# Kernel optimization log

Measured on AMD Instinct MI355X. Metric: run time of the kernel, lower is better.

Reference implementation:

```python
import jax, jax.numpy as jnp
import numpy as np

N_NODES = 50000
N_EDGES = 800000
IN_DIM = 128
HID_DIM = 128
OUT_DIM = 64


def setup_inputs() -> dict:
    key = jax.random.key(0)
    ks = jax.random.split(key, 6)
    x = jax.random.normal(ks[0], (N_NODES, IN_DIM), dtype=jnp.float32)
    edge_index = jax.random.randint(ks[1], (2, N_EDGES), 0, N_NODES, dtype=jnp.int64)
    # per-hop linear weights (torch Linear layout: [out, in], no bias)
    s = 1.0 / np.sqrt(IN_DIM)
    W0 = jax.random.uniform(ks[2], (HID_DIM, IN_DIM), jnp.float32, -s, s)
    W1 = jax.random.uniform(ks[3], (HID_DIM, IN_DIM), jnp.float32, -s, s)
    W2 = jax.random.uniform(ks[4], (HID_DIM, IN_DIM), jnp.float32, -s, s)
    s2 = 1.0 / np.sqrt(HID_DIM * 3)
    Wfc = jax.random.uniform(ks[5], (OUT_DIM, HID_DIM * 3), jnp.float32, -s2, s2)
    return {"x": x, "edge_index": edge_index, "W0": W0, "W1": W1, "W2": W2, "Wfc": Wfc}


def reference(x, edge_index, W0, W1, W2, Wfc):
    N = x.shape[0]
    row, col = edge_index[0], edge_index[1]  # source, target (PyG source_to_target flow)
    # symmetric degree normalization based on in-degree (degree(col, N))
    deg = jax.ops.segment_sum(jnp.ones(row.shape[0], dtype=x.dtype), col, num_segments=N)
    deg_inv_sqrt = jnp.where(deg > 0, jax.lax.rsqrt(jnp.where(deg > 0, deg, 1.0)), 0.0)
    norm = deg_inv_sqrt[row] * deg_inv_sqrt[col]  # [E]
    # NOTE: original code propagates the ORIGINAL x each iteration, so hops 1 and 2
    # both see the 1-hop propagation of x. Faithfully reproduced here.
    px = jax.ops.segment_sum(norm[:, None] * x[row], col, num_segments=N)  # [N, IN_DIM]
    # per-hop linear projections, concat over hops p=[0,1,2]
    h = jnp.concatenate([x @ W0.T, px @ W1.T, px @ W2.T], axis=1)  # [N, 3*HID_DIM]
    return h @ Wfc.T  # [N, OUT_DIM]
```

## Files before the change

kernel.cpp:

```cpp
#include <hip/hip_runtime.h>
#include <hip/hip_bf16.h>

#define N_IN  128
#define N_OUT 64
#define CFB    256
#define MAXNBC 200
#define SLACKC 5120
#define CHUNK  2048
#define PADR   136

typedef __attribute__((ext_vector_type(8))) short short8;
typedef __attribute__((ext_vector_type(4))) float floatx4;

__device__ __forceinline__ unsigned pack_bf16(float a, float b) {
    __hip_bfloat16 ba = __float2bfloat16(a);
    __hip_bfloat16 bb = __float2bfloat16(b);
    unsigned short ua = *(unsigned short*)&ba;
    unsigned short ub = *(unsigned short*)&bb;
    return ((unsigned)ub << 16) | ua;
}
__device__ __forceinline__ float blo(unsigned u) { return __uint_as_float(u << 16); }
__device__ __forceinline__ float bhi(unsigned u) { return __uint_as_float(u & 0xffff0000u); }

__global__ void prep_kernel(const float* __restrict__ W0,
                            const float* __restrict__ W1,
                            const float* __restrict__ W2,
                            const float* __restrict__ Wfc,
                            __hip_bfloat16* __restrict__ CT,
                            int* __restrict__ gcur, int NBC) {
    int t = blockIdx.x * blockDim.x + threadIdx.x;
    if (t < NBC) gcur[t] = t * SLACKC;
    if (t >= 128 * 128) return;
    int n = t >> 7;
    int i = t & 127;
    float a = 0.f;
    if (n < 64) {
        for (int k = 0; k < 128; ++k)
            a += Wfc[n * 384 + k] * W0[k * N_IN + i];
    } else {
        int o = n - 64;
        for (int k = 0; k < 128; ++k)
            a += Wfc[o * 384 + 128 + k] * W1[k * N_IN + i]
               + Wfc[o * 384 + 256 + k] * W2[k * N_IN + i];
    }
    CT[t] = __float2bfloat16(a);
}

__global__ __launch_bounds__(256) void fill_scatter(const int* __restrict__ ei,
                                                    int* __restrict__ gcur,
                                                    unsigned* __restrict__ gsorted,
                                                    int E, int NBC) {
    __shared__ int lcnt[MAXNBC];
    __shared__ int gbase_s[MAXNBC];
    int base = blockIdx.x * CHUNK;
    for (int i = threadIdx.x; i < NBC; i += 256) lcnt[i] = 0;
    __syncthreads();
    int myc[CHUNK / 256];
    #pragma unroll
    for (int q = 0; q < CHUNK / 256; ++q) {
        int e = base + q * 256 + threadIdx.x;
        int c = (e < E) ? ei[E + e] : -1;
        myc[q] = c;
        if (c >= 0) atomicAdd(&lcnt[c >> 8], 1);
    }
    __syncthreads();
    for (int f = threadIdx.x; f < NBC; f += 256) {
        int n = lcnt[f];
        gbase_s[f] = (n > 0) ? atomicAdd(&gcur[f], n) : 0;
    }
    __syncthreads();
    #pragma unroll
    for (int q = 0; q < CHUNK / 256; ++q) {
        int c = myc[q];
        if (c >= 0) {
            int e = base + q * 256 + threadIdx.x;
            unsigned r = (unsigned)ei[e];
            int p = atomicAdd(&gbase_s[c >> 8], 1);
            if (p < ((c >> 8) + 1) * SLACKC)
                gsorted[p] = ((unsigned)c << 16) | r;
        }
    }
}

__global__ __launch_bounds__(256) void sortgemm_kernel(
        const int* __restrict__ gcur,
        const unsigned* __restrict__ gsorted,
        unsigned short* __restrict__ srow,
        int* __restrict__ offs,
        int* __restrict__ cnt,
        float* __restrict__ dis,
        const float* __restrict__ x,
        const __hip_bfloat16* __restrict__ CT,
        float* __restrict__ out,
        __hip_bfloat16* __restrict__ z,
        int N, int NBC) {
    __shared__ __align__(16) char smem[(64 + 128) * PADR * 2];
    int tid = threadIdx.x;

    if (blockIdx.x < NBC) {
        unsigned* ev = (unsigned*)smem;
        int* c256 = (int*)(smem + SLACKC * 4);
        int* cur  = c256 + 256;
        int* ts   = cur + 256;
        int f = blockIdx.x;
        int lo = f * SLACKC;
        int m = min(gcur[f] - lo, SLACKC);
        for (int i = tid; i < m; i += 256) ev[i] = gsorted[lo + i];
        c256[tid] = 0;
        __syncthreads();
        for (int i = tid; i < m; i += 256)
            atomicAdd(&c256[(ev[i] >> 16) & (CFB - 1)], 1);
        __syncthreads();
        int v = c256[tid];
        int xx = v;
        ts[tid] = xx;
        __syncthreads();
        for (int off = 1; off < 256; off <<= 1) {
            int t2 = (tid >= off) ? ts[tid - off] : 0;
            __syncthreads();
            xx += t2; ts[tid] = xx;
            __syncthreads();
        }
        int b = xx - v;
        cur[tid] = b;
        int node = f * CFB + tid;
        if (node < N) {
            offs[node] = lo + b;
            cnt[node] = v;
            dis[node] = v > 0 ? rsqrtf((float)v) : 0.f;
        }
        __syncthreads();
        for (int i = tid; i < m; i += 256) {
            unsigned val = ev[i];
            int cl = (val >> 16) & (CFB - 1);
            int p = atomicAdd(&cur[cl], 1);
            srow[lo + p] = (unsigned short)(val & 0xffffu);
        }
        return;
    }

    unsigned short* xs = (unsigned short*)smem;
    unsigned short* Bs = xs + 64 * PADR;
    int base = (blockIdx.x - NBC) * 64;

    {
        int row = tid >> 2;
        int colq = (tid & 3) * 32;
        int node = base + row;
        unsigned tmp[16];
        if (node < N) {
            const float4* src = (const float4*)(x + (size_t)node * N_IN + colq);
            #pragma unroll
            for (int q = 0; q < 8; ++q) {
                float4 v = src[q];
                tmp[q * 2]     = pack_bf16(v.x, v.y);
                tmp[q * 2 + 1] = pack_bf16(v.z, v.w);
            }
        } else {
            #pragma unroll
            for (int q = 0; q < 16; ++q) tmp[q] = 0u;
        }
        unsigned* dst = (unsigned*)(xs + row * PADR + colq);
        #pragma unroll
        for (int q = 0; q < 16; ++q) dst[q] = tmp[q];
    }
    {
        const unsigned* src = (const unsigned*)CT;
        for (int c = tid; c < 8192; c += 256) {
            int row = c >> 6;
            int col = (c & 63) * 2;
            *(unsigned*)(Bs + row * PADR + col) = src[c];
        }
    }
    __syncthreads();

    int wave = tid >> 6, lane = tid & 63;
    int wm = wave & 1, wn = wave >> 1;
    int quad = lane >> 4, l16 = lane & 15;

    floatx4 acc[2][4];
    #pragma unroll
    for (int mt = 0; mt < 2; ++mt)
        #pragma unroll
        for (int nt = 0; nt < 4; ++nt)
            acc[mt][nt] = (floatx4){0.f, 0.f, 0.f, 0.f};

    #pragma unroll
    for (int kc = 0; kc < 4; ++kc) {
        int kof = kc * 32 + quad * 8;
        short8 afr[2], bfr[4];
        #pragma unroll
        for (int mt = 0; mt < 2; ++mt)
            afr[mt] = *(const short8*)(xs + (wm * 32 + mt * 16 + l16) * PADR + kof);
        #pragma unroll
        for (int nt = 0; nt < 4; ++nt)
            bfr[nt] = *(const short8*)(Bs + (wn * 64 + nt * 16 + l16) * PADR + kof);
        #pragma unroll
        for (int mt = 0; mt < 2; ++mt)
            #pragma unroll
            for (int nt = 0; nt < 4; ++nt)
                acc[mt][nt] = __builtin_amdgcn_mfma_f32_16x16x32_bf16(
                    afr[mt], bfr[nt], acc[mt][nt], 0, 0, 0);
    }

    #pragma unroll
    for (int mt = 0; mt < 2; ++mt) {
        #pragma unroll
        for (int reg = 0; reg < 4; ++reg) {
            int node = base + wm * 32 + mt * 16 + quad * 4 + reg;
            if (node >= N) continue;
            if (wn == 0) {
                #pragma unroll
                for (int nt = 0; nt < 4; ++nt)
                    out[(size_t)node * N_OUT + nt * 16 + l16] = acc[mt][nt][reg];
            } else {
                #pragma unroll
                for (int nt = 0; nt < 4; ++nt)
                    z[((size_t)node << 6) + nt * 16 + l16] =
                        __float2bfloat16(acc[mt][nt][reg]);
            }
        }
    }
}

__global__ __launch_bounds__(256) void gather_kernel(
        const int* __restrict__ offs, const int* __restrict__ cnt,
        const unsigned short* __restrict__ srow, const __hip_bfloat16* __restrict__ z,
        const float* __restrict__ dis, float* __restrict__ out, int N) {
    int node = blockIdx.x * 4 + (threadIdx.x >> 6);
    if (node >= N) return;
    int lane = threadIdx.x & 63;
    int sub  = lane >> 3;
    int jj   = lane & 7;
    int start = offs[node];
    int deg   = cnt[node];
    float a[8] = {0.f, 0.f, 0.f, 0.f, 0.f, 0.f, 0.f, 0.f};
    for (int k0 = 0; k0 < deg; k0 += 64) {
        int m = min(64, deg - k0);
        int idx = 0; float dv = 0.f;
        if (lane < m) {
            idx = (int)srow[start + k0 + lane];
            dv = dis[idx];
        }
        for (int kk = 0; kk < m; kk += 16) {
            int s0 = kk + sub, s1 = kk + 8 + sub;
            int r0 = __shfl(idx, s0); float d0 = __shfl(dv, s0);
            int r1 = __shfl(idx, s1); float d1 = __shfl(dv, s1);
            uint4 u0 = make_uint4(0u, 0u, 0u, 0u), u1 = make_uint4(0u, 0u, 0u, 0u);
            if (s0 < m) u0 = ((const uint4*)(z + ((size_t)r0 << 6)))[jj];
            if (s1 < m) u1 = ((const uint4*)(z + ((size_t)r1 << 6)))[jj];
            a[0] += d0 * blo(u0.x) + d1 * blo(u1.x);
            a[1] += d0 * bhi(u0.x) + d1 * bhi(u1.x);
            a[2] += d0 * blo(u0.y) + d1 * blo(u1.y);
            a[3] += d0 * bhi(u0.y) + d1 * bhi(u1.y);
            a[4] += d0 * blo(u0.z) + d1 * blo(u1.z);
            a[5] += d0 * bhi(u0.z) + d1 * bhi(u1.z);
            a[6] += d0 * blo(u0.w) + d1 * blo(u1.w);
            a[7] += d0 * bhi(u0.w) + d1 * bhi(u1.w);
        }
    }
    #pragma unroll
    for (int q = 0; q < 8; ++q) {
        a[q] += __shfl_xor(a[q], 8);
        a[q] += __shfl_xor(a[q], 16);
        a[q] += __shfl_xor(a[q], 32);
    }
    if (lane < 8 && deg > 0) {
        float dn = dis[node];
        float4* op = (float4*)(out + ((size_t)node << 6) + jj * 8);
        float4 o0 = op[0], o1 = op[1];
        o0.x += dn * a[0]; o0.y += dn * a[1]; o0.z += dn * a[2]; o0.w += dn * a[3];
        o1.x += dn * a[4]; o1.y += dn * a[5]; o1.z += dn * a[6]; o1.w += dn * a[7];
        op[0] = o0; op[1] = o1;
    }
}

extern "C" void kernel_launch(void* const* d_in, const int* in_sizes, int n_in,
                              void* d_out, int out_size, void* d_ws, size_t ws_size,
                              hipStream_t stream) {
    const float* x   = (const float*)d_in[0];
    const int*   ei  = (const int*)d_in[1];
    const float* W0  = (const float*)d_in[2];
    const float* W1  = (const float*)d_in[3];
    const float* W2  = (const float*)d_in[4];
    const float* Wfc = (const float*)d_in[5];
    float* out = (float*)d_out;
    int N = in_sizes[0] / N_IN;
    int E = in_sizes[1] / 2;
    int NBC = (N + CFB - 1) / CFB;
    int GB  = (N + 63) / 64;

    __hip_bfloat16* CT = (__hip_bfloat16*)d_ws;
    int*   cnt     = (int*)((char*)d_ws + 32768);
    float* dis     = (float*)(cnt + N);
    int*   gcur    = (int*)(dis + N);
    int*   offs    = gcur + NBC;
    unsigned* gsorted = (unsigned*)(offs + N);
    unsigned short* srow = (unsigned short*)(gsorted + (size_t)NBC * SLACKC);
    size_t zoff = ((size_t)(srow + (size_t)NBC * SLACKC) - (size_t)d_ws + 15) & ~(size_t)15;
    __hip_bfloat16* z = (__hip_bfloat16*)((char*)d_ws + zoff);

    prep_kernel<<<64, 256, 0, stream>>>(W0, W1, W2, Wfc, CT, gcur, NBC);
    fill_scatter<<<(E + CHUNK - 1) / CHUNK, 256, 0, stream>>>(ei, gcur, gsorted, E, NBC);
    sortgemm_kernel<<<NBC + GB, 256, 0, stream>>>(gcur, gsorted, srow, offs, cnt, dis,
                                                  x, CT, out, z, N, NBC);
    gather_kernel<<<(N + 3) / 4, 256, 0, stream>>>(offs, cnt, srow, z, dis, out, N);
}
```

Baseline: 148.0 us.

## Store propagated features as FP8 and fold weight prep into scatter kernel

After: 144.5 us (median of 2 runs). 2.4% less time.

```diff
diff --git a/kernel.cpp b/kernel.cpp
--- a/kernel.cpp
+++ b/kernel.cpp
@@ -11,6 +11,7 @@
 
 typedef __attribute__((ext_vector_type(8))) short short8;
 typedef __attribute__((ext_vector_type(4))) float floatx4;
+typedef __attribute__((ext_vector_type(2))) float floatx2;
 
 __device__ __forceinline__ unsigned pack_bf16(float a, float b) {
     __hip_bfloat16 ba = __float2bfloat16(a);
@@ -19,36 +20,18 @@
     unsigned short ub = *(unsigned short*)&bb;
     return ((unsigned)ub << 16) | ua;
 }
-__device__ __forceinline__ float blo(unsigned u) { return __uint_as_float(u << 16); }
-__device__ __forceinline__ float bhi(unsigned u) { return __uint_as_float(u & 0xffff0000u); }
-
-__global__ void prep_kernel(const float* __restrict__ W0,
-                            const float* __restrict__ W1,
-                            const float* __restrict__ W2,
-                            const float* __restrict__ Wfc,
-                            __hip_bfloat16* __restrict__ CT,
-                            int* __restrict__ gcur, int NBC) {
-    int t = blockIdx.x * blockDim.x + threadIdx.x;
-    if (t < NBC) gcur[t] = t * SLACKC;
-    if (t >= 128 * 128) return;
-    int n = t >> 7;
-    int i = t & 127;
-    float a = 0.f;
-    if (n < 64) {
-        for (int k = 0; k < 128; ++k)
-            a += Wfc[n * 384 + k] * W0[k * N_IN + i];
-    } else {
-        int o = n - 64;
-        for (int k = 0; k < 128; ++k)
-            a += Wfc[o * 384 + 128 + k] * W1[k * N_IN + i]
-               + Wfc[o * 384 + 256 + k] * W2[k * N_IN + i];
-    }
-    CT[t] = __float2bfloat16(a);
+__device__ __forceinline__ unsigned char fp8b(float v) {
+    return (unsigned char)(__builtin_amdgcn_cvt_pk_fp8_f32(v, v, 0, false) & 0xff);
 }
 
 __global__ __launch_bounds__(256) void fill_scatter(const int* __restrict__ ei,
                                                     int* __restrict__ gcur,
                                                     unsigned* __restrict__ gsorted,
+                                                    const float* __restrict__ W0,
+                                                    const float* __restrict__ W1,
+                                                    const float* __restrict__ W2,
+                                                    const float* __restrict__ Wfc,
+                                                    __hip_bfloat16* __restrict__ CT,
                                                     int E, int NBC) {
     __shared__ int lcnt[MAXNBC];
     __shared__ int gbase_s[MAXNBC];
@@ -66,7 +49,7 @@
     __syncthreads();
     for (int f = threadIdx.x; f < NBC; f += 256) {
         int n = lcnt[f];
-        gbase_s[f] = (n > 0) ? atomicAdd(&gcur[f], n) : 0;
+        gbase_s[f] = (n > 0) ? (f * SLACKC + atomicAdd(&gcur[f], n)) : 0;
     }
     __syncthreads();
     #pragma unroll
@@ -79,6 +62,22 @@
             if (p < ((c >> 8) + 1) * SLACKC)
                 gsorted[p] = ((unsigned)c << 16) | r;
         }
+    }
+    if (blockIdx.x < 64) {
+        int t = blockIdx.x * 256 + threadIdx.x;
+        int n = t >> 7;
+        int i = t & 127;
+        float a = 0.f;
+        if (n < 64) {
+            for (int k = 0; k < 128; ++k)
+                a += Wfc[n * 384 + k] * W0[k * N_IN + i];
+        } else {
+            int o = n - 64;
+            for (int k = 0; k < 128; ++k)
+                a += Wfc[o * 384 + 128 + k] * W1[k * N_IN + i]
+                   + Wfc[o * 384 + 256 + k] * W2[k * N_IN + i];
+        }
+        CT[t] = __float2bfloat16(a);
     }
 }
 
@@ -92,7 +91,7 @@
         const float* __restrict__ x,
         const __hip_bfloat16* __restrict__ CT,
         float* __restrict__ out,
-        __hip_bfloat16* __restrict__ z,
+        unsigned char* __restrict__ z8,
         int N, int NBC) {
     __shared__ __align__(16) char smem[(64 + 128) * PADR * 2];
     int tid = threadIdx.x;
@@ -104,7 +103,7 @@
         int* ts   = cur + 256;
         int f = blockIdx.x;
         int lo = f * SLACKC;
-        int m = min(gcur[f] - lo, SLACKC);
+        int m = min(gcur[f], SLACKC);
         for (int i = tid; i < m; i += 256) ev[i] = gsorted[lo + i];
         c256[tid] = 0;
         __syncthreads();
@@ -216,8 +215,7 @@
             } else {
                 #pragma unroll
                 for (int nt = 0; nt < 4; ++nt)
-                    z[((size_t)node << 6) + nt * 16 + l16] =
-                        __float2bfloat16(acc[mt][nt][reg]);
+                    z8[((size_t)node << 6) + nt * 16 + l16] = fp8b(acc[mt][nt][reg]);
             }
         }
     }
@@ -225,7 +223,7 @@
 
 __global__ __launch_bounds__(256) void gather_kernel(
         const int* __restrict__ offs, const int* __restrict__ cnt,
-        const unsigned short* __restrict__ srow, const __hip_bfloat16* __restrict__ z,
+        const unsigned short* __restrict__ srow, const unsigned char* __restrict__ z8,
         const float* __restrict__ dis, float* __restrict__ out, int N) {
     int node = blockIdx.x * 4 + (threadIdx.x >> 6);
     if (node >= N) return;
@@ -246,17 +244,25 @@
             int s0 = kk + sub, s1 = kk + 8 + sub;
             int r0 = __shfl(idx, s0); float d0 = __shfl(dv, s0);
             int r1 = __shfl(idx, s1); float d1 = __shfl(dv, s1);
-            uint4 u0 = make_uint4(0u, 0u, 0u, 0u), u1 = make_uint4(0u, 0u, 0u, 0u);
-            if (s0 < m) u0 = ((const uint4*)(z + ((size_t)r0 << 6)))[jj];
-            if (s1 < m) u1 = ((const uint4*)(z + ((size_t)r1 << 6)))[jj];
-            a[0] += d0 * blo(u0.x) + d1 * blo(u1.x);
-            a[1] += d0 * bhi(u0.x) + d1 * bhi(u1.x);
-            a[2] += d0 * blo(u0.y) + d1 * blo(u1.y);
-            a[3] += d0 * bhi(u0.y) + d1 * bhi(u1.y);
-            a[4] += d0 * blo(u0.z) + d1 * blo(u1.z);
-            a[5] += d0 * bhi(u0.z) + d1 * bhi(u1.z);
-            a[6] += d0 * blo(u0.w) + d1 * blo(u1.w);
-            a[7] += d0 * bhi(u0.w) + d1 * bhi(u1.w);
+            uint2 u0 = make_uint2(0u, 0u), u1 = make_uint2(0u, 0u);
+            if (s0 < m) u0 = *(const uint2*)(z8 + ((size_t)r0 << 6) + jj * 8);
+            if (s1 < m) u1 = *(const uint2*)(z8 + ((size_t)r1 << 6) + jj * 8);
+            floatx2 p00 = __builtin_amdgcn_cvt_pk_f32_fp8(u0.x, false);
+            floatx2 p01 = __builtin_amdgcn_cvt_pk_f32_fp8(u0.x, true);
+            floatx2 p02 = __builtin_amdgcn_cvt_pk_f32_fp8(u0.y, false);
+            floatx2 p03 = __builtin_amdgcn_cvt_pk_f32_fp8(u0.y, true);
+            floatx2 p10 = __builtin_amdgcn_cvt_pk_f32_fp8(u1.x, false);
+            floatx2 p11 = __builtin_amdgcn_cvt_pk_f32_fp8(u1.x, true);
+            floatx2 p12 = __builtin_amdgcn_cvt_pk_f32_fp8(u1.y, false);
+            floatx2 p13 = __builtin_amdgcn_cvt_pk_f32_fp8(u1.y, true);
+            a[0] += d0 * p00.x + d1 * p10.x;
+            a[1] += d0 * p00.y + d1 * p10.y;
+            a[2] += d0 * p01.x + d1 * p11.x;
+            a[3] += d0 * p01.y + d1 * p11.y;
+            a[4] += d0 * p02.x + d1 * p12.x;
+            a[5] += d0 * p02.y + d1 * p12.y;
+            a[6] += d0 * p03.x + d1 * p13.x;
+            a[7] += d0 * p03.y + d1 * p13.y;
         }
     }
     #pragma unroll
@@ -297,12 +303,13 @@
     int*   offs    = gcur + NBC;
     unsigned* gsorted = (unsigned*)(offs + N);
     unsigned short* srow = (unsigned short*)(gsorted + (size_t)NBC * SLACKC);
-    size_t zoff = ((size_t)(srow + (size_t)NBC * SLACKC) - (size_t)d_ws + 15) & ~(size_t)15;
-    __hip_bfloat16* z = (__hip_bfloat16*)((char*)d_ws + zoff);
-
-    prep_kernel<<<64, 256, 0, stream>>>(W0, W1, W2, Wfc, CT, gcur, NBC);
-    fill_scatter<<<(E + CHUNK - 1) / CHUNK, 256, 0, stream>>>(ei, gcur, gsorted, E, NBC);
+    size_t zoff = ((size_t)(srow + (size_t)NBC * SLACKC) - (size_t)d_ws + 63) & ~(size_t)63;
+    unsigned char* z8 = (unsigned char*)d_ws + zoff;
+
+    hipMemsetAsync(gcur, 0, (size_t)NBC * sizeof(int), stream);
+    fill_scatter<<<(E + CHUNK - 1) / CHUNK, 256, 0, stream>>>(ei, gcur, gsorted,
+                                                              W0, W1, W2, Wfc, CT, E, NBC);
     sortgemm_kernel<<<NBC + GB, 256, 0, stream>>>(gcur, gsorted, srow, offs, cnt, dis,
-                                                  x, CT, out, z, N, NBC);
-    gather_kernel<<<(N + 3) / 4, 256, 0, stream>>>(offs, cnt, srow, z, dis, out, N);
-}
+                                                  x, CT, out, z8, N, NBC);
+    gather_kernel<<<(N + 3) / 4, 256, 0, stream>>>(offs, cnt, srow, z8, dis, out, N);
+}
```
